# Kernel tuning notes

Hardware: AMD Instinct MI355X
Metric: run time of the kernel (lower is better)

The kernel has to match this reference:

```python
import jax, jax.numpy as jnp
import numpy as np

B, S, H, D = 256, 512, 256, 512  # batch, n_seq, n_hid, n_dim
LN_EPS = 1e-5


def _xavier(key, fan_out, fan_in):
    lim = (6.0 / (fan_in + fan_out)) ** 0.5
    return jax.random.uniform(key, (fan_out, fan_in), jnp.float32, -lim, lim)


def setup_inputs() -> dict:
    key = jax.random.key(0)
    ks = jax.random.split(key, 10)
    x = jax.random.normal(ks[0], (B, S, D), jnp.float32)
    k_w = _xavier(ks[1], H, D)
    q_w = _xavier(ks[2], H, D)
    v_w = _xavier(ks[3], H, D)
    lb = 1.0 / (D ** 0.5)
    k_b = jax.random.uniform(ks[4], (H,), jnp.float32, -lb, lb)
    q_b = jax.random.uniform(ks[5], (H,), jnp.float32, -lb, lb)
    v_b = jax.random.uniform(ks[6], (H,), jnp.float32, -lb, lb)
    attn_bias = jax.random.normal(ks[7], (S, H), jnp.float32)
    ln_g = jnp.ones((H,), jnp.float32)
    ln_b = jnp.zeros((H,), jnp.float32)
    lo = 1.0 / ((S * H) ** 0.5)
    out_w = jax.random.uniform(ks[8], (D, S * H), jnp.float32, -lo, lo)
    out_b = jax.random.uniform(ks[9], (D,), jnp.float32, -lo, lo)
    return {"x": x, "k_w": k_w, "k_b": k_b, "q_w": q_w, "q_b": q_b,
            "v_w": v_w, "v_b": v_b, "attn_bias": attn_bias,
            "ln_g": ln_g, "ln_b": ln_b, "out_w": out_w, "out_b": out_b}


def reference(x, k_w, k_b, q_w, q_b, v_w, v_b, attn_bias, ln_g, ln_b, out_w, out_b):
    # projections: [B,S,D] -> [B,S,H]
    k = jnp.einsum('bsd,hd->bsh', x, k_w) + k_b
    q = jnp.einsum('bsd,hd->bsh', x, q_w) + q_b
    v = jnp.einsum('bsd,hd->bsh', x, v_w) + v_b
    # scores = k^T q, scaled by BATCH size^-0.5 (faithful to v.shape[0]**-0.5)
    scale = x.shape[0] ** (-0.5)
    scores = jnp.einsum('bsh,bsg->bhg', k, q) * scale  # [B,H,H]
    weight = jax.nn.softmax(scores, axis=1)
    out = jnp.einsum('bsh,bhg->bsg', v, weight)  # [B,S,H]
    out = out + attn_bias
    # LayerNorm over last dim
    mu = out.mean(-1, keepdims=True)
    var = out.var(-1, keepdims=True)
    out = (out - mu) * jax.lax.rsqrt(var + LN_EPS) * ln_g + ln_b
    # dropout is identity in eval mode; exact (erf) GELU matches torch default
    out = jax.nn.gelu(out, approximate=False)
    out = out.reshape(out.shape[0], S * H)
    out = out @ out_w.T + out_b  # [B,D]
    return out[:, None, :]  # [B,1,D]
```

## Files before the change

kernel.cpp:

```cpp
#include <hip/hip_runtime.h>
#include <hip/hip_bf16.h>
#include <math.h>

#define B_ 256
#define S_ 512
#define H_ 256
#define D_ 512

typedef __bf16 bf16;
typedef __bf16 bf16x8 __attribute__((ext_vector_type(8)));
typedef float  f32x4  __attribute__((ext_vector_type(4)));
typedef unsigned short u16x8 __attribute__((ext_vector_type(8)));
typedef unsigned short u16x4 __attribute__((ext_vector_type(4)));

#define MFMA(a, b, c) __builtin_amdgcn_mfma_f32_16x16x32_bf16((a), (b), (c), 0, 0, 0)

__device__ __forceinline__ int swz(int row, int kbyte) {
  return (row * 128 + kbyte) ^ ((row & 7) << 4);
}
__device__ __forceinline__ int pswz(int row, int kbyte) {
  return (row * 512 + kbyte) ^ ((row & 7) << 4);
}
__device__ __forceinline__ unsigned short bfbits(float f) {
  bf16 h = (bf16)f;
  union { bf16 b; unsigned short u; } c; c.b = h; return c.u;
}
__device__ __forceinline__ bf16x8 cvt8(const float* __restrict__ p) {
  f32x4 a = *(const f32x4*)p;
  f32x4 b = *(const f32x4*)(p + 4);
  bf16x8 r;
  r[0] = (bf16)a[0]; r[1] = (bf16)a[1]; r[2] = (bf16)a[2]; r[3] = (bf16)a[3];
  r[4] = (bf16)b[0]; r[5] = (bf16)b[1]; r[6] = (bf16)b[2]; r[7] = (bf16)b[3];
  return r;
}
__device__ __forceinline__ void gload16(const unsigned short* g, unsigned char* l) {
  __builtin_amdgcn_global_load_lds(
      (const __attribute__((address_space(1))) unsigned int*)g,
      (__attribute__((address_space(3))) unsigned int*)l, 16, 0, 0);
}

__global__ __launch_bounds__(256) void k_convw(
    const float* __restrict__ kw, const float* __restrict__ qw,
    const float* __restrict__ vw, unsigned short* __restrict__ wc)
{
  const int r = blockIdx.x;
  const float* src = (r < 256) ? kw + (size_t)r * 512
                   : (r < 512) ? qw + (size_t)(r - 256) * 512
                               : vw + (size_t)(r - 512) * 512;
  const int c = threadIdx.x * 2;
  wc[(size_t)r * 512 + c]     = bfbits(src[c]);
  wc[(size_t)r * 512 + c + 1] = bfbits(src[c + 1]);
}

__global__ __launch_bounds__(256) void k_convx(
    const float* __restrict__ x, unsigned short* __restrict__ xb, int nchunk)
{
  for (int c = blockIdx.x * 256 + threadIdx.x; c < nchunk; c += gridDim.x * 256) {
    bf16x8 v = cvt8(x + (size_t)c * 8);
    *(bf16x8*)(xb + (size_t)c * 8) = v;
  }
}

__global__ __launch_bounds__(256) void k_proj2(
    const unsigned short* __restrict__ xb,
    const unsigned short* __restrict__ wc,
    const float* __restrict__ kbi, const float* __restrict__ qbi,
    const float* __restrict__ vbi,
    unsigned short* __restrict__ k_t, unsigned short* __restrict__ q_t,
    unsigned short* __restrict__ v_o, int cstart, int nwg)
{
  __shared__ __align__(16) unsigned char sA[16384];
  __shared__ __align__(16) unsigned char sB[16384];

  const int o = blockIdx.x;
  const int cpx = nwg >> 3;
  const int a = (o & 7) * cpx + (o >> 3);
  const int mt = a / 6;
  const int nb = a - mt * 6;
  const int m0 = mt * 128;
  const int n0 = nb * 128;
  const int region = nb >> 1;
  const int h0 = (nb & 1) * 128;
  const float* __restrict__ Bi = (region == 0) ? kbi : (region == 1) ? qbi : vbi;

  const int tid = threadIdx.x;
  const int lane = tid & 63;
  const int wid = tid >> 6;
  const int wm = wid >> 1;
  const int wn = wid & 1;

  f32x4 acc[4][4];
#pragma unroll
  for (int i = 0; i < 4; ++i)
#pragma unroll
    for (int j = 0; j < 4; ++j) acc[i][j] = (f32x4){0.f, 0.f, 0.f, 0.f};

  const int lr = lane >> 3;
  const int lk = (lane & 7) << 3;

  for (int kt = 0; kt < 8; ++kt) {
    if (kt) __syncthreads();
#pragma unroll
    for (int i = 0; i < 4; ++i) {
      const int chunk = wid * 4 + i;
      const int row = chunk * 8 + lr;
      gload16(xb + (size_t)(m0 + row) * 512 + kt * 64 + lk, sA + chunk * 1024);
      gload16(wc + (size_t)(n0 + row) * 512 + kt * 64 + lk, sB + chunk * 1024);
    }
    __syncthreads();
#pragma unroll
    for (int ks = 0; ks < 2; ++ks) {
      const int kb2 = ks * 64 + ((lane >> 4) << 4);
      bf16x8 av[4], bv[4];
#pragma unroll
      for (int f = 0; f < 4; ++f)
        av[f] = *(const bf16x8*)(sA + (wm * 64 + f * 16 + (lane & 15)) * 128 + kb2);
#pragma unroll
      for (int f = 0; f < 4; ++f)
        bv[f] = *(const bf16x8*)(sB + (wn * 64 + f * 16 + (lane & 15)) * 128 + kb2);
#pragma unroll
      for (int fm = 0; fm < 4; ++fm)
#pragma unroll
        for (int fn = 0; fn < 4; ++fn)
          acc[fm][fn] = MFMA(av[fm], bv[fn], acc[fm][fn]);
    }
  }

  const int m0g = cstart * 512 + m0;
  const int b = m0g >> 9;
  const int sbase = m0g & 511;
  const int r4 = (lane >> 4) * 4;
#pragma unroll
  for (int fn = 0; fn < 4; ++fn) {
    const int hcol = h0 + wn * 64 + fn * 16 + (lane & 15);
    const float bias = Bi[hcol];
#pragma unroll
    for (int fm = 0; fm < 4; ++fm) {
      const int s = sbase + wm * 64 + fm * 16 + r4;
      if (region < 2) {
        unsigned short* dst = ((region == 0) ? k_t : q_t) +
                              (size_t)b * (H_ * S_) + (size_t)hcol * S_ + s;
        u16x4 ov;
#pragma unroll
        for (int j = 0; j < 4; ++j) ov[j] = bfbits(acc[fm][fn][j] + bias);
        *(u16x4*)dst = ov;
      } else {
#pragma unroll
        for (int j = 0; j < 4; ++j)
          v_o[(size_t)b * (S_ * H_) + (size_t)(s + j) * H_ + hcol] =
              bfbits(acc[fm][fn][j] + bias);
      }
    }
  }
}

__global__ __launch_bounds__(512, 2) void k_attn(
    const unsigned short* __restrict__ k_t,
    const unsigned short* __restrict__ q_t,
    const unsigned short* __restrict__ v_o,
    const float* __restrict__ attn_bias,
    const float* __restrict__ lng, const float* __restrict__ lnb,
    unsigned short* __restrict__ act)
{
  __shared__ __align__(16) unsigned char sP[131072];
  __shared__ float lbuf[2][4][128];

  const int tid = threadIdx.x;
  const int lane = tid & 63;
  const int wid = tid >> 6;
  const int b = blockIdx.x;
  const int l15 = lane & 15;
  const int l16 = lane >> 4;
  const int r4 = l16 * 4;

  const unsigned short* __restrict__ Kb = k_t + (size_t)b * (H_ * S_);
  const unsigned short* __restrict__ Qb = q_t + (size_t)b * (H_ * S_);
  const unsigned short* __restrict__ Vb = v_o + (size_t)b * (S_ * H_);

  unsigned char* sK = sP;
  unsigned char* sQ = sP + 32768;
  float* redm = (float*)(sP + 65536);
  float* reds = (float*)(sP + 67584);

  const int wh = wid >> 2;
  const int wg = wid & 3;

  f32x4 acc1[8][4];
#pragma unroll
  for (int i = 0; i < 8; ++i)
#pragma unroll
    for (int j = 0; j < 4; ++j) acc1[i][j] = (f32x4){0.f, 0.f, 0.f, 0.f};

  for (int kt = 0; kt < 8; ++kt) {
    __syncthreads();
#pragma unroll
    for (int i = 0; i < 4; ++i) {
      int c = tid + i * 512;
      int row = c >> 3, kc = (c & 7) * 8;
      *(u16x8*)(sK + swz(row, kc * 2)) =
          *(const u16x8*)(Kb + (size_t)row * S_ + kt * 64 + kc);
      *(u16x8*)(sQ + swz(row, kc * 2)) =
          *(const u16x8*)(Qb + (size_t)row * S_ + kt * 64 + kc);
    }
    __syncthreads();
#pragma unroll
    for (int ks = 0; ks < 2; ++ks) {
      const int kbyte = ks * 64 + l16 * 16;
      bf16x8 av[8], bv[4];
#pragma unroll
      for (int f = 0; f < 8; ++f)
        av[f] = *(const bf16x8*)(sK + swz(wh * 128 + f * 16 + l15, kbyte));
#pragma unroll
      for (int f = 0; f < 4; ++f)
        bv[f] = *(const bf16x8*)(sQ + swz(wg * 64 + f * 16 + l15, kbyte));
#pragma unroll
      for (int fm = 0; fm < 8; ++fm)
#pragma unroll
        for (int fn = 0; fn < 4; ++fn)
          acc1[fm][fn] = MFMA(av[fm], bv[fn], acc1[fm][fn]);
    }
  }

#pragma unroll
  for (int fm = 0; fm < 8; ++fm)
#pragma unroll
    for (int fn = 0; fn < 4; ++fn)
#pragma unroll
      for (int j = 0; j < 4; ++j) acc1[fm][fn][j] *= 0.0625f;

  float cmax[4] = {-3.0e38f, -3.0e38f, -3.0e38f, -3.0e38f};
#pragma unroll
  for (int fm = 0; fm < 8; ++fm)
#pragma unroll
    for (int fn = 0; fn < 4; ++fn)
#pragma unroll
      for (int j = 0; j < 4; ++j) cmax[fn] = fmaxf(cmax[fn], acc1[fm][fn][j]);
#pragma unroll
  for (int fn = 0; fn < 4; ++fn) {
    cmax[fn] = fmaxf(cmax[fn], __shfl_xor(cmax[fn], 16));
    cmax[fn] = fmaxf(cmax[fn], __shfl_xor(cmax[fn], 32));
  }
  if (lane < 16) {
#pragma unroll
    for (int fn = 0; fn < 4; ++fn)
      redm[wh * 256 + wg * 64 + fn * 16 + lane] = cmax[fn];
  }
  __syncthreads();
  float gmax[4];
#pragma unroll
  for (int fn = 0; fn < 4; ++fn) {
    int c = wg * 64 + fn * 16 + l15;
    gmax[fn] = fmaxf(redm[c], redm[256 + c]);
  }
  float csum[4] = {0.f, 0.f, 0.f, 0.f};
#pragma unroll
  for (int fm = 0; fm < 8; ++fm)
#pragma unroll
    for (int fn = 0; fn < 4; ++fn)
#pragma unroll
      for (int j = 0; j < 4; ++j) {
        float p = __expf(acc1[fm][fn][j] - gmax[fn]);
        acc1[fm][fn][j] = p;
        csum[fn] += p;
      }
#pragma unroll
  for (int fn = 0; fn < 4; ++fn) {
    csum[fn] += __shfl_xor(csum[fn], 16);
    csum[fn] += __shfl_xor(csum[fn], 32);
  }
  if (lane < 16) {
#pragma unroll
    for (int fn = 0; fn < 4; ++fn)
      reds[wh * 256 + wg * 64 + fn * 16 + lane] = csum[fn];
  }
  __syncthreads();
  float ginv[4];
#pragma unroll
  for (int fn = 0; fn < 4; ++fn) {
    int c = wg * 64 + fn * 16 + l15;
    ginv[fn] = 1.0f / (reds[c] + reds[256 + c]);
  }
  __syncthreads();

#pragma unroll
  for (int fn = 0; fn < 4; ++fn) {
    const int g = wg * 64 + fn * 16 + l15;
#pragma unroll
    for (int fm = 0; fm < 8; ++fm) {
      const int h = wh * 128 + fm * 16 + r4;
      u16x4 pv;
#pragma unroll
      for (int j = 0; j < 4; ++j) pv[j] = bfbits(acc1[fm][fn][j] * ginv[fn]);
      *(u16x4*)(sP + pswz(g, h * 2)) = pv;
    }
  }
  __syncthreads();

  const float* __restrict__ bias = attn_bias;
  for (int ms = 0; ms < 4; ++ms) {
    const int s0 = ms * 128 + wh * 64;
    f32x4 acc2[4][4];
#pragma unroll
    for (int i = 0; i < 4; ++i)
#pragma unroll
      for (int j = 0; j < 4; ++j) acc2[i][j] = (f32x4){0.f, 0.f, 0.f, 0.f};

#pragma unroll
    for (int kt = 0; kt < 4; ++kt) {
      bf16x8 av[4][2];
#pragma unroll
      for (int fm = 0; fm < 4; ++fm)
#pragma unroll
        for (int ks = 0; ks < 2; ++ks)
          av[fm][ks] = *(const bf16x8*)(
              Vb + (size_t)(s0 + fm * 16 + l15) * H_ + kt * 64 + ks * 32 + l16 * 8);
#pragma unroll
      for (int ks = 0; ks < 2; ++ks) {
        bf16x8 bv[4];
#pragma unroll
        for (int fn = 0; fn < 4; ++fn)
          bv[fn] = *(const bf16x8*)(
              sP + pswz(wg * 64 + fn * 16 + l15, kt * 128 + ks * 64 + l16 * 16));
#pragma unroll
        for (int fm = 0; fm < 4; ++fm)
#pragma unroll
          for (int fn = 0; fn < 4; ++fn)
            acc2[fm][fn] = MFMA(av[fm][ks], bv[fn], acc2[fm][fn]);
      }
    }

    __syncthreads();
#pragma unroll
    for (int fm = 0; fm < 4; ++fm) {
#pragma unroll
      for (int j = 0; j < 4; ++j) {
        const int rloc = wh * 64 + fm * 16 + r4 + j;
        const int s = ms * 128 + rloc;
        float ps = 0.f, psq = 0.f;
#pragma unroll
        for (int fn = 0; fn < 4; ++fn) {
          int g = wg * 64 + fn * 16 + l15;
          float vv = acc2[fm][fn][j] + bias[(size_t)s * H_ + g];
          acc2[fm][fn][j] = vv;
          ps += vv; psq += vv * vv;
        }
        ps += __shfl_xor(ps, 1);  psq += __shfl_xor(psq, 1);
        ps += __shfl_xor(ps, 2);  psq += __shfl_xor(psq, 2);
        ps += __shfl_xor(ps, 4);  psq += __shfl_xor(psq, 4);
        ps += __shfl_xor(ps, 8);  psq += __shfl_xor(psq, 8);
        if (l15 == 0) { lbuf[0][wg][rloc] = ps; lbuf[1][wg][rloc] = psq; }
      }
    }
    __syncthreads();
#pragma unroll
    for (int fm = 0; fm < 4; ++fm) {
#pragma unroll
      for (int j = 0; j < 4; ++j) {
        const int rloc = wh * 64 + fm * 16 + r4 + j;
        const int s = ms * 128 + rloc;
        float sum = lbuf[0][0][rloc] + lbuf[0][1][rloc] + lbuf[0][2][rloc] + lbuf[0][3][rloc];
        float sq  = lbuf[1][0][rloc] + lbuf[1][1][rloc] + lbuf[1][2][rloc] + lbuf[1][3][rloc];
        float mu = sum * (1.f / H_);
        float var = sq * (1.f / H_) - mu * mu;
        float rstd = rsqrtf(var + 1e-5f);
#pragma unroll
        for (int fn = 0; fn < 4; ++fn) {
          int g = wg * 64 + fn * 16 + l15;
          float xv = (acc2[fm][fn][j] - mu) * rstd * lng[g] + lnb[g];
          float y = 0.5f * xv * (1.f + erff(xv * 0.70710678118654752f));
          act[(size_t)b * (S_ * H_) + (size_t)s * H_ + g] = bfbits(y);
        }
      }
    }
  }
}

__global__ __launch_bounds__(512) void k_final(
    const unsigned short* __restrict__ act,
    const float* __restrict__ ow,
    float* __restrict__ partial)
{
  __shared__ __align__(16) unsigned char sA[256 * 128];
  __shared__ __align__(16) unsigned char sB[64 * 128];

  const int tid = threadIdx.x;
  const int lane = tid & 63;
  const int wid = tid >> 6;
  const int wm = wid >> 1;
  const int wn = wid & 1;
  const int n0 = blockIdx.x * 64;
  const size_t k0 = (size_t)blockIdx.y * 4096;

  f32x4 acc[4][2];
#pragma unroll
  for (int i = 0; i < 4; ++i)
#pragma unroll
    for (int j = 0; j < 2; ++j) acc[i][j] = (f32x4){0.f, 0.f, 0.f, 0.f};

  for (int kt = 0; kt < 64; ++kt) {
    const size_t kb = k0 + kt * 64;
    __syncthreads();
#pragma unroll
    for (int i = 0; i < 4; ++i) {
      int c = tid + i * 512;
      int row = c >> 3, kc = (c & 7) * 8;
      *(u16x8*)(sA + swz(row, kc * 2)) =
          *(const u16x8*)(act + (size_t)row * 131072 + kb + kc);
    }
    {
      int row = tid >> 3, kc = (tid & 7) * 8;
      *(bf16x8*)(sB + swz(row, kc * 2)) =
          cvt8(ow + (size_t)(n0 + row) * 131072 + kb + kc);
    }
    __syncthreads();
#pragma unroll
    for (int ks = 0; ks < 2; ++ks) {
      const int kbyte = ks * 64 + (lane >> 4) * 16;
      bf16x8 av[4], bv[2];
#pragma unroll
      for (int f = 0; f < 4; ++f)
        av[f] = *(const bf16x8*)(sA + swz(wm * 64 + f * 16 + (lane & 15), kbyte));
#pragma unroll
      for (int f = 0; f < 2; ++f)
        bv[f] = *(const bf16x8*)(sB + swz(wn * 32 + f * 16 + (lane & 15), kbyte));
#pragma unroll
      for (int fm = 0; fm < 4; ++fm)
#pragma unroll
        for (int fn = 0; fn < 2; ++fn)
          acc[fm][fn] = MFMA(av[fm], bv[fn], acc[fm][fn]);
    }
  }

  float* __restrict__ P = partial + (size_t)blockIdx.y * (256 * 512);
  const int r4 = (lane >> 4) * 4;
#pragma unroll
  for (int fn = 0; fn < 2; ++fn) {
    int col = n0 + wn * 32 + fn * 16 + (lane & 15);
#pragma unroll
    for (int fm = 0; fm < 4; ++fm) {
      int mb = wm * 64 + fm * 16 + r4;
#pragma unroll
      for (int j = 0; j < 4; ++j)
        P[(size_t)(mb + j) * 512 + col] = acc[fm][fn][j];
    }
  }
}

__global__ __launch_bounds__(256) void k_reduce(
    const float* __restrict__ partial,
    const float* __restrict__ ob,
    float* __restrict__ out)
{
  const int i4 = blockIdx.x * 256 + threadIdx.x;
  f32x4 s = *(const f32x4*)(ob + ((i4 & 127) << 2));
#pragma unroll
  for (int ks = 0; ks < 32; ++ks)
    s += *(const f32x4*)(partial + (size_t)ks * 131072 + (size_t)i4 * 4);
  *(f32x4*)(out + (size_t)i4 * 4) = s;
}

extern "C" void kernel_launch(void* const* d_in, const int* in_sizes, int n_in,
                              void* d_out, int out_size, void* d_ws, size_t ws_size,
                              hipStream_t stream) {
  const float* x         = (const float*)d_in[0];
  const float* k_w       = (const float*)d_in[1];
  const float* k_b       = (const float*)d_in[2];
  const float* q_w       = (const float*)d_in[3];
  const float* q_b       = (const float*)d_in[4];
  const float* v_w       = (const float*)d_in[5];
  const float* v_b       = (const float*)d_in[6];
  const float* attn_bias = (const float*)d_in[7];
  const float* ln_g      = (const float*)d_in[8];
  const float* ln_b      = (const float*)d_in[9];
  const float* out_w     = (const float*)d_in[10];
  const float* out_b     = (const float*)d_in[11];
  float* out = (float*)d_out;

  char* ws = (char*)d_ws;
  unsigned short* k_t = (unsigned short*)(ws);
  unsigned short* q_t = (unsigned short*)(ws + 67108864);
  unsigned short* v_o = (unsigned short*)(ws + 134217728);
  unsigned short* wc  = (unsigned short*)(ws + 201326592);
  unsigned short* xb  = (unsigned short*)(ws + 201326592 + 786432);
  unsigned short* act = k_t;
  float* partial      = (float*)(ws + 67108864);

  k_convw<<<dim3(768), dim3(256), 0, stream>>>(k_w, q_w, v_w, wc);

  const int starts[5] = {0, 56, 112, 168, 224};
  const int nbats[5]  = {56, 56, 56, 56, 32};
  for (int r = 0; r < 5; ++r) {
    const int nbat = nbats[r];
    k_convx<<<dim3(1024), dim3(256), 0, stream>>>(
        x + (size_t)starts[r] * 262144, xb, nbat * 32768);
    const int nwg = nbat * 24;
    k_proj2<<<dim3(nwg), dim3(256), 0, stream>>>(
        xb, wc, k_b, q_b, v_b, k_t, q_t, v_o, starts[r], nwg);
  }

  k_attn<<<dim3(256), dim3(512), 0, stream>>>(
      k_t, q_t, v_o, attn_bias, ln_g, ln_b, act);

  k_final<<<dim3(8, 32), dim3(512), 0, stream>>>(act, out_w, partial);
  k_reduce<<<dim3(128), dim3(256), 0, stream>>>(partial, out_b, out);
}
```

Before: 517.8 us.

## Fuse x bf16 conversion into projection GEMM and restructure attention kernel

The separate x-to-bf16 conversion kernel and the five chunked projection launches are replaced by a single projection launch that reads fp32 x, converts it to bf16 in registers and stores it into swizzled LDS. The attention kernel is rewritten so each wave owns 32 full score columns, reading K and Q directly from global memory without LDS staging. Softmax reductions now stay inside each wave, and the probability matrix is handed to the second MFMA stage through lane shuffles instead of a 128KB LDS buffer. This removes an intermediate buffer round-trip, several launches and many block barriers, but repeats the fp32 x load and conversion across the six N-tiles and drops LDS reuse of K and V.

```diff
diff --git a/kernel.cpp b/kernel.cpp
--- a/kernel.cpp
+++ b/kernel.cpp
@@ -12,14 +12,12 @@
 typedef float  f32x4  __attribute__((ext_vector_type(4)));
 typedef unsigned short u16x8 __attribute__((ext_vector_type(8)));
 typedef unsigned short u16x4 __attribute__((ext_vector_type(4)));
+typedef unsigned int   u32x4 __attribute__((ext_vector_type(4)));
 
 #define MFMA(a, b, c) __builtin_amdgcn_mfma_f32_16x16x32_bf16((a), (b), (c), 0, 0, 0)
 
 __device__ __forceinline__ int swz(int row, int kbyte) {
   return (row * 128 + kbyte) ^ ((row & 7) << 4);
-}
-__device__ __forceinline__ int pswz(int row, int kbyte) {
-  return (row * 512 + kbyte) ^ ((row & 7) << 4);
 }
 __device__ __forceinline__ unsigned short bfbits(float f) {
   bf16 h = (bf16)f;
@@ -52,22 +50,13 @@
   wc[(size_t)r * 512 + c + 1] = bfbits(src[c + 1]);
 }
 
-__global__ __launch_bounds__(256) void k_convx(
-    const float* __restrict__ x, unsigned short* __restrict__ xb, int nchunk)
-{
-  for (int c = blockIdx.x * 256 + threadIdx.x; c < nchunk; c += gridDim.x * 256) {
-    bf16x8 v = cvt8(x + (size_t)c * 8);
-    *(bf16x8*)(xb + (size_t)c * 8) = v;
-  }
-}
-
 __global__ __launch_bounds__(256) void k_proj2(
-    const unsigned short* __restrict__ xb,
+    const float* __restrict__ x,
     const unsigned short* __restrict__ wc,
     const float* __restrict__ kbi, const float* __restrict__ qbi,
     const float* __restrict__ vbi,
     unsigned short* __restrict__ k_t, unsigned short* __restrict__ q_t,
-    unsigned short* __restrict__ v_o, int cstart, int nwg)
+    unsigned short* __restrict__ v_o, int nwg)
 {
   __shared__ __align__(16) unsigned char sA[16384];
   __shared__ __align__(16) unsigned char sB[16384];
@@ -88,6 +77,7 @@
   const int wid = tid >> 6;
   const int wm = wid >> 1;
   const int wn = wid & 1;
+  const int l15 = lane & 15;
 
   f32x4 acc[4][4];
 #pragma unroll
@@ -100,11 +90,17 @@
 
   for (int kt = 0; kt < 8; ++kt) {
     if (kt) __syncthreads();
+#pragma unroll
+    for (int i = 0; i < 4; ++i) {
+      int c = tid + i * 256;
+      int row = c >> 3, kc = (c & 7) * 8;
+      *(bf16x8*)(sA + swz(row, kc * 2)) =
+          cvt8(x + (size_t)(m0 + row) * D_ + kt * 64 + kc);
+    }
 #pragma unroll
     for (int i = 0; i < 4; ++i) {
       const int chunk = wid * 4 + i;
       const int row = chunk * 8 + lr;
-      gload16(xb + (size_t)(m0 + row) * 512 + kt * 64 + lk, sA + chunk * 1024);
       gload16(wc + (size_t)(n0 + row) * 512 + kt * 64 + lk, sB + chunk * 1024);
     }
     __syncthreads();
@@ -114,10 +110,10 @@
       bf16x8 av[4], bv[4];
 #pragma unroll
       for (int f = 0; f < 4; ++f)
-        av[f] = *(const bf16x8*)(sA + (wm * 64 + f * 16 + (lane & 15)) * 128 + kb2);
+        av[f] = *(const bf16x8*)(sA + swz(wm * 64 + f * 16 + l15, kb2));
 #pragma unroll
       for (int f = 0; f < 4; ++f)
-        bv[f] = *(const bf16x8*)(sB + (wn * 64 + f * 16 + (lane & 15)) * 128 + kb2);
+        bv[f] = *(const bf16x8*)(sB + (wn * 64 + f * 16 + l15) * 128 + kb2);
 #pragma unroll
       for (int fm = 0; fm < 4; ++fm)
 #pragma unroll
@@ -126,13 +122,12 @@
     }
   }
 
-  const int m0g = cstart * 512 + m0;
-  const int b = m0g >> 9;
-  const int sbase = m0g & 511;
+  const int b = m0 >> 9;
+  const int sbase = m0 & 511;
   const int r4 = (lane >> 4) * 4;
 #pragma unroll
   for (int fn = 0; fn < 4; ++fn) {
-    const int hcol = h0 + wn * 64 + fn * 16 + (lane & 15);
+    const int hcol = h0 + wn * 64 + fn * 16 + l15;
     const float bias = Bi[hcol];
 #pragma unroll
     for (int fm = 0; fm < 4; ++fm) {
@@ -162,188 +157,156 @@
     const float* __restrict__ lng, const float* __restrict__ lnb,
     unsigned short* __restrict__ act)
 {
-  __shared__ __align__(16) unsigned char sP[131072];
-  __shared__ float lbuf[2][4][128];
+  __shared__ float lbuf[2][8][64];
 
   const int tid = threadIdx.x;
   const int lane = tid & 63;
-  const int wid = tid >> 6;
+  const int wg = tid >> 6;
   const int b = blockIdx.x;
   const int l15 = lane & 15;
   const int l16 = lane >> 4;
-  const int r4 = l16 * 4;
+  const int g0 = wg * 32;
 
   const unsigned short* __restrict__ Kb = k_t + (size_t)b * (H_ * S_);
   const unsigned short* __restrict__ Qb = q_t + (size_t)b * (H_ * S_);
   const unsigned short* __restrict__ Vb = v_o + (size_t)b * (S_ * H_);
 
-  unsigned char* sK = sP;
-  unsigned char* sQ = sP + 32768;
-  float* redm = (float*)(sP + 65536);
-  float* reds = (float*)(sP + 67584);
-
-  const int wh = wid >> 2;
-  const int wg = wid & 3;
-
-  f32x4 acc1[8][4];
-#pragma unroll
-  for (int i = 0; i < 8; ++i)
-#pragma unroll
-    for (int j = 0; j < 4; ++j) acc1[i][j] = (f32x4){0.f, 0.f, 0.f, 0.f};
+  f32x4 acc1[16][2];
+#pragma unroll
+  for (int i = 0; i < 16; ++i) {
+    acc1[i][0] = (f32x4){0.f, 0.f, 0.f, 0.f};
+    acc1[i][1] = (f32x4){0.f, 0.f, 0.f, 0.f};
+  }
 
   for (int kt = 0; kt < 8; ++kt) {
-    __syncthreads();
+#pragma unroll
+    for (int ks = 0; ks < 2; ++ks) {
+      const int soff = kt * 64 + ks * 32 + l16 * 8;
+      bf16x8 bv0 = *(const bf16x8*)(Qb + (size_t)(g0 + l15) * S_ + soff);
+      bf16x8 bv1 = *(const bf16x8*)(Qb + (size_t)(g0 + 16 + l15) * S_ + soff);
+#pragma unroll
+      for (int fh = 0; fh < 2; ++fh) {
+        bf16x8 av[8];
+#pragma unroll
+        for (int f = 0; f < 8; ++f)
+          av[f] = *(const bf16x8*)(Kb + (size_t)((fh * 8 + f) * 16 + l15) * S_ + soff);
+#pragma unroll
+        for (int f = 0; f < 8; ++f) {
+          acc1[fh * 8 + f][0] = MFMA(av[f], bv0, acc1[fh * 8 + f][0]);
+          acc1[fh * 8 + f][1] = MFMA(av[f], bv1, acc1[fh * 8 + f][1]);
+        }
+      }
+    }
+  }
+
+  float mx[2] = {-3.0e38f, -3.0e38f};
+#pragma unroll
+  for (int fm = 0; fm < 16; ++fm)
+#pragma unroll
+    for (int fn = 0; fn < 2; ++fn)
+#pragma unroll
+      for (int j = 0; j < 4; ++j) {
+        acc1[fm][fn][j] *= 0.0625f;
+        mx[fn] = fmaxf(mx[fn], acc1[fm][fn][j]);
+      }
+#pragma unroll
+  for (int fn = 0; fn < 2; ++fn) {
+    mx[fn] = fmaxf(mx[fn], __shfl_xor(mx[fn], 16));
+    mx[fn] = fmaxf(mx[fn], __shfl_xor(mx[fn], 32));
+  }
+  float sm[2] = {0.f, 0.f};
+#pragma unroll
+  for (int fm = 0; fm < 16; ++fm)
+#pragma unroll
+    for (int fn = 0; fn < 2; ++fn)
+#pragma unroll
+      for (int j = 0; j < 4; ++j) {
+        float p = __expf(acc1[fm][fn][j] - mx[fn]);
+        acc1[fm][fn][j] = p;
+        sm[fn] += p;
+      }
+  float gi[2];
+#pragma unroll
+  for (int fn = 0; fn < 2; ++fn) {
+    sm[fn] += __shfl_xor(sm[fn], 16);
+    sm[fn] += __shfl_xor(sm[fn], 32);
+    gi[fn] = 1.0f / sm[fn];
+  }
+
+  bf16x8 bvv[8][2];
+  const int src0 = l15 + ((l16 & 1) << 5);
+  const int src1 = src0 + 16;
+  const bool hi = (l16 >> 1) != 0;
+#pragma unroll
+  for (int kb = 0; kb < 8; ++kb) {
+#pragma unroll
+    for (int fn = 0; fn < 2; ++fn) {
+      const float gi_ = gi[fn];
+      unsigned int A0 = bfbits(acc1[kb * 2][fn][0] * gi_) |
+                        ((unsigned int)bfbits(acc1[kb * 2][fn][1] * gi_) << 16);
+      unsigned int A1 = bfbits(acc1[kb * 2][fn][2] * gi_) |
+                        ((unsigned int)bfbits(acc1[kb * 2][fn][3] * gi_) << 16);
+      unsigned int B0 = bfbits(acc1[kb * 2 + 1][fn][0] * gi_) |
+                        ((unsigned int)bfbits(acc1[kb * 2 + 1][fn][1] * gi_) << 16);
+      unsigned int B1 = bfbits(acc1[kb * 2 + 1][fn][2] * gi_) |
+                        ((unsigned int)bfbits(acc1[kb * 2 + 1][fn][3] * gi_) << 16);
+      unsigned int t0 = (unsigned int)__shfl((int)A0, src0);
+      unsigned int t1 = (unsigned int)__shfl((int)A1, src0);
+      unsigned int t2 = (unsigned int)__shfl((int)A0, src1);
+      unsigned int t3 = (unsigned int)__shfl((int)A1, src1);
+      unsigned int u0 = (unsigned int)__shfl((int)B0, src0);
+      unsigned int u1 = (unsigned int)__shfl((int)B1, src0);
+      unsigned int u2 = (unsigned int)__shfl((int)B0, src1);
+      unsigned int u3 = (unsigned int)__shfl((int)B1, src1);
+      u32x4 w;
+      w[0] = hi ? u0 : t0;
+      w[1] = hi ? u1 : t1;
+      w[2] = hi ? u2 : t2;
+      w[3] = hi ? u3 : t3;
+      union { u32x4 u; bf16x8 v; } cv;
+      cv.u = w;
+      bvv[kb][fn] = cv.v;
+    }
+  }
+
+  __syncthreads();
+
+  const float lgm0 = lng[g0 + l15],      lbm0 = lnb[g0 + l15];
+  const float lgm1 = lng[g0 + 16 + l15], lbm1 = lnb[g0 + 16 + l15];
+
+  for (int ms = 0; ms < 8; ++ms) {
+    const int s0 = ms * 64;
+    f32x4 acc2[4][2];
 #pragma unroll
     for (int i = 0; i < 4; ++i) {
-      int c = tid + i * 512;
-      int row = c >> 3, kc = (c & 7) * 8;
-      *(u16x8*)(sK + swz(row, kc * 2)) =
-          *(const u16x8*)(Kb + (size_t)row * S_ + kt * 64 + kc);
-      *(u16x8*)(sQ + swz(row, kc * 2)) =
-          *(const u16x8*)(Qb + (size_t)row * S_ + kt * 64 + kc);
-    }
-    __syncthreads();
-#pragma unroll
-    for (int ks = 0; ks < 2; ++ks) {
-      const int kbyte = ks * 64 + l16 * 16;
-      bf16x8 av[8], bv[4];
-#pragma unroll
-      for (int f = 0; f < 8; ++f)
-        av[f] = *(const bf16x8*)(sK + swz(wh * 128 + f * 16 + l15, kbyte));
+      acc2[i][0] = (f32x4){0.f, 0.f, 0.f, 0.f};
+      acc2[i][1] = (f32x4){0.f, 0.f, 0.f, 0.f};
+    }
+#pragma unroll
+    for (int kb = 0; kb < 8; ++kb) {
+      bf16x8 av[4];
 #pragma unroll
       for (int f = 0; f < 4; ++f)
-        bv[f] = *(const bf16x8*)(sQ + swz(wg * 64 + f * 16 + l15, kbyte));
-#pragma unroll
-      for (int fm = 0; fm < 8; ++fm)
-#pragma unroll
-        for (int fn = 0; fn < 4; ++fn)
-          acc1[fm][fn] = MFMA(av[fm], bv[fn], acc1[fm][fn]);
-    }
-  }
-
-#pragma unroll
-  for (int fm = 0; fm < 8; ++fm)
-#pragma unroll
-    for (int fn = 0; fn < 4; ++fn)
-#pragma unroll
-      for (int j = 0; j < 4; ++j) acc1[fm][fn][j] *= 0.0625f;
-
-  float cmax[4] = {-3.0e38f, -3.0e38f, -3.0e38f, -3.0e38f};
-#pragma unroll
-  for (int fm = 0; fm < 8; ++fm)
-#pragma unroll
-    for (int fn = 0; fn < 4; ++fn)
-#pragma unroll
-      for (int j = 0; j < 4; ++j) cmax[fn] = fmaxf(cmax[fn], acc1[fm][fn][j]);
-#pragma unroll
-  for (int fn = 0; fn < 4; ++fn) {
-    cmax[fn] = fmaxf(cmax[fn], __shfl_xor(cmax[fn], 16));
-    cmax[fn] = fmaxf(cmax[fn], __shfl_xor(cmax[fn], 32));
-  }
-  if (lane < 16) {
-#pragma unroll
-    for (int fn = 0; fn < 4; ++fn)
-      redm[wh * 256 + wg * 64 + fn * 16 + lane] = cmax[fn];
-  }
-  __syncthreads();
-  float gmax[4];
-#pragma unroll
-  for (int fn = 0; fn < 4; ++fn) {
-    int c = wg * 64 + fn * 16 + l15;
-    gmax[fn] = fmaxf(redm[c], redm[256 + c]);
-  }
-  float csum[4] = {0.f, 0.f, 0.f, 0.f};
-#pragma unroll
-  for (int fm = 0; fm < 8; ++fm)
-#pragma unroll
-    for (int fn = 0; fn < 4; ++fn)
+        av[f] = *(const bf16x8*)(
+            Vb + (size_t)(s0 + f * 16 + l15) * H_ + kb * 32 + l16 * 8);
+#pragma unroll
+      for (int f = 0; f < 4; ++f) {
+        acc2[f][0] = MFMA(av[f], bvv[kb][0], acc2[f][0]);
+        acc2[f][1] = MFMA(av[f], bvv[kb][1], acc2[f][1]);
+      }
+    }
+
+#pragma unroll
+    for (int f = 0; f < 4; ++f) {
 #pragma unroll
       for (int j = 0; j < 4; ++j) {
-        float p = __expf(acc1[fm][fn][j] - gmax[fn]);
-        acc1[fm][fn][j] = p;
-        csum[fn] += p;
-      }
-#pragma unroll
-  for (int fn = 0; fn < 4; ++fn) {
-    csum[fn] += __shfl_xor(csum[fn], 16);
-    csum[fn] += __shfl_xor(csum[fn], 32);
-  }
-  if (lane < 16) {
-#pragma unroll
-    for (int fn = 0; fn < 4; ++fn)
-      reds[wh * 256 + wg * 64 + fn * 16 + lane] = csum[fn];
-  }
-  __syncthreads();
-  float ginv[4];
-#pragma unroll
-  for (int fn = 0; fn < 4; ++fn) {
-    int c = wg * 64 + fn * 16 + l15;
-    ginv[fn] = 1.0f / (reds[c] + reds[256 + c]);
-  }
-  __syncthreads();
-
-#pragma unroll
-  for (int fn = 0; fn < 4; ++fn) {
-    const int g = wg * 64 + fn * 16 + l15;
-#pragma unroll
-    for (int fm = 0; fm < 8; ++fm) {
-      const int h = wh * 128 + fm * 16 + r4;
-      u16x4 pv;
-#pragma unroll
-      for (int j = 0; j < 4; ++j) pv[j] = bfbits(acc1[fm][fn][j] * ginv[fn]);
-      *(u16x4*)(sP + pswz(g, h * 2)) = pv;
-    }
-  }
-  __syncthreads();
-
-  const float* __restrict__ bias = attn_bias;
-  for (int ms = 0; ms < 4; ++ms) {
-    const int s0 = ms * 128 + wh * 64;
-    f32x4 acc2[4][4];
-#pragma unroll
-    for (int i = 0; i < 4; ++i)
-#pragma unroll
-      for (int j = 0; j < 4; ++j) acc2[i][j] = (f32x4){0.f, 0.f, 0.f, 0.f};
-
-#pragma unroll
-    for (int kt = 0; kt < 4; ++kt) {
-      bf16x8 av[4][2];
-#pragma unroll
-      for (int fm = 0; fm < 4; ++fm)
-#pragma unroll
-        for (int ks = 0; ks < 2; ++ks)
-          av[fm][ks] = *(const bf16x8*)(
-              Vb + (size_t)(s0 + fm * 16 + l15) * H_ + kt * 64 + ks * 32 + l16 * 8);
-#pragma unroll
-      for (int ks = 0; ks < 2; ++ks) {
-        bf16x8 bv[4];
-#pragma unroll
-        for (int fn = 0; fn < 4; ++fn)
-          bv[fn] = *(const bf16x8*)(
-              sP + pswz(wg * 64 + fn * 16 + l15, kt * 128 + ks * 64 + l16 * 16));
-#pragma unroll
-        for (int fm = 0; fm < 4; ++fm)
-#pragma unroll
-          for (int fn = 0; fn < 4; ++fn)
-            acc2[fm][fn] = MFMA(av[fm][ks], bv[fn], acc2[fm][fn]);
-      }
-    }
-
-    __syncthreads();
-#pragma unroll
-    for (int fm = 0; fm < 4; ++fm) {
-#pragma unroll
-      for (int j = 0; j < 4; ++j) {
-        const int rloc = wh * 64 + fm * 16 + r4 + j;
-        const int s = ms * 128 + rloc;
-        float ps = 0.f, psq = 0.f;
-#pragma unroll
-        for (int fn = 0; fn < 4; ++fn) {
-          int g = wg * 64 + fn * 16 + l15;
-          float vv = acc2[fm][fn][j] + bias[(size_t)s * H_ + g];
-          acc2[fm][fn][j] = vv;
-          ps += vv; psq += vv * vv;
-        }
+        const int rloc = f * 16 + l16 * 4 + j;
+        const int s = s0 + rloc;
+        float v0 = acc2[f][0][j] + attn_bias[(size_t)s * H_ + g0 + l15];
+        float v1 = acc2[f][1][j] + attn_bias[(size_t)s * H_ + g0 + 16 + l15];
+        acc2[f][0][j] = v0;
+        acc2[f][1][j] = v1;
+        float ps = v0 + v1, psq = v0 * v0 + v1 * v1;
         ps += __shfl_xor(ps, 1);  psq += __shfl_xor(psq, 1);
         ps += __shfl_xor(ps, 2);  psq += __shfl_xor(psq, 2);
         ps += __shfl_xor(ps, 4);  psq += __shfl_xor(psq, 4);
@@ -353,25 +316,26 @@
     }
     __syncthreads();
 #pragma unroll
-    for (int fm = 0; fm < 4; ++fm) {
+    for (int f = 0; f < 4; ++f) {
 #pragma unroll
       for (int j = 0; j < 4; ++j) {
-        const int rloc = wh * 64 + fm * 16 + r4 + j;
-        const int s = ms * 128 + rloc;
-        float sum = lbuf[0][0][rloc] + lbuf[0][1][rloc] + lbuf[0][2][rloc] + lbuf[0][3][rloc];
-        float sq  = lbuf[1][0][rloc] + lbuf[1][1][rloc] + lbuf[1][2][rloc] + lbuf[1][3][rloc];
+        const int rloc = f * 16 + l16 * 4 + j;
+        const int s = s0 + rloc;
+        float sum = 0.f, sq = 0.f;
+#pragma unroll
+        for (int w = 0; w < 8; ++w) { sum += lbuf[0][w][rloc]; sq += lbuf[1][w][rloc]; }
         float mu = sum * (1.f / H_);
         float var = sq * (1.f / H_) - mu * mu;
         float rstd = rsqrtf(var + 1e-5f);
-#pragma unroll
-        for (int fn = 0; fn < 4; ++fn) {
-          int g = wg * 64 + fn * 16 + l15;
-          float xv = (acc2[fm][fn][j] - mu) * rstd * lng[g] + lnb[g];
-          float y = 0.5f * xv * (1.f + erff(xv * 0.70710678118654752f));
-          act[(size_t)b * (S_ * H_) + (size_t)s * H_ + g] = bfbits(y);
-        }
-      }
-    }
+        float x0 = (acc2[f][0][j] - mu) * rstd * lgm0 + lbm0;
+        float x1 = (acc2[f][1][j] - mu) * rstd * lgm1 + lbm1;
+        float y0 = 0.5f * x0 * (1.f + erff(x0 * 0.70710678118654752f));
+        float y1 = 0.5f * x1 * (1.f + erff(x1 * 0.70710678118654752f));
+        act[(size_t)b * (S_ * H_) + (size_t)s * H_ + g0 + l15] = bfbits(y0);
+        act[(size_t)b * (S_ * H_) + (size_t)s * H_ + g0 + 16 + l15] = bfbits(y1);
+      }
+    }
+    __syncthreads();
   }
 }
 
@@ -481,22 +445,14 @@
   unsigned short* q_t = (unsigned short*)(ws + 67108864);
   unsigned short* v_o = (unsigned short*)(ws + 134217728);
   unsigned short* wc  = (unsigned short*)(ws + 201326592);
-  unsigned short* xb  = (unsigned short*)(ws + 201326592 + 786432);
   unsigned short* act = k_t;
   float* partial      = (float*)(ws + 67108864);
 
   k_convw<<<dim3(768), dim3(256), 0, stream>>>(k_w, q_w, v_w, wc);
 
-  const int starts[5] = {0, 56, 112, 168, 224};
-  const int nbats[5]  = {56, 56, 56, 56, 32};
-  for (int r = 0; r < 5; ++r) {
-    const int nbat = nbats[r];
-    k_convx<<<dim3(1024), dim3(256), 0, stream>>>(
-        x + (size_t)starts[r] * 262144, xb, nbat * 32768);
-    const int nwg = nbat * 24;
-    k_proj2<<<dim3(nwg), dim3(256), 0, stream>>>(
-        xb, wc, k_b, q_b, v_b, k_t, q_t, v_o, starts[r], nwg);
-  }
+  const int nwg = 6144;
+  k_proj2<<<dim3(nwg), dim3(256), 0, stream>>>(
+      x, wc, k_b, q_b, v_b, k_t, q_t, v_o, nwg);
 
   k_attn<<<dim3(256), dim3(512), 0, stream>>>(
       k_t, q_t, v_o, attn_bias, ln_g, ln_b, act);
```

New measurement: 582.6 us. 1.13x slower.
